# Kernel optimization log

Measured on AMD Instinct MI355X. Metric: run time of the kernel, lower is better.

## Reference

```python
import jax, jax.numpy as jnp
import numpy as np

C = 256
C8 = C // 8


def setup_inputs() -> dict:
    key = jax.random.key(0)
    ks = jax.random.split(key, 9)
    B, H, W = 4, 64, 64
    s = 1.0 / np.sqrt(C)
    return {
        "pre_feat": jax.random.normal(ks[0], (B, C, H, W), jnp.float32),
        "post_feat": jax.random.normal(ks[1], (B, C, H, W), jnp.float32),
        "Wq": jax.random.normal(ks[2], (C8, C), jnp.float32) * s,
        "bq": jnp.zeros((C8,), jnp.float32),
        "Wk": jax.random.normal(ks[3], (C8, C), jnp.float32) * s,
        "bk": jnp.zeros((C8,), jnp.float32),
        "Wv": jax.random.normal(ks[4], (C, C), jnp.float32) * s,
        "bv": jnp.zeros((C,), jnp.float32),
        "gamma": jnp.zeros((1,), jnp.float32),
    }


def reference(pre_feat, post_feat, Wq, bq, Wk, bk, Wv, bv, gamma):
    B, Cc, H, W = pre_feat.shape
    N = H * W
    pre = pre_feat.reshape(B, Cc, N)    # (B, C, N)
    post = post_feat.reshape(B, Cc, N)
    # 1x1 convs == per-pixel linear projections
    q = jnp.einsum('dc,bcn->bdn', Wq, post) + bq[None, :, None]  # (B, C8, N)
    k = jnp.einsum('dc,bcn->bdn', Wk, pre) + bk[None, :, None]   # (B, C8, N)
    v = jnp.einsum('dc,bcn->bdn', Wv, pre) + bv[None, :, None]   # (B, C, N)
    # energy[b,i,j] = <q[b,:,i], k[b,:,j]>  (unscaled)
    energy = jnp.einsum('bdi,bdj->bij', q, k)                    # (B, N, N)
    attention = jax.nn.softmax(energy, axis=-1)
    # out[b,c,i] = sum_j v[b,c,j] * attention[b,i,j]
    out = jnp.einsum('bcj,bij->bci', v, attention).reshape(B, Cc, H, W)
    return gamma[0] * out + post_feat
```

## Files before the change

kernel.cpp:

```cpp
#include <hip/hip_runtime.h>
#include <hip/hip_bf16.h>

#define Bn 4
#define Cn 256
#define Dn 32
#define Nn 4096

typedef __bf16 bf16x8 __attribute__((ext_vector_type(8)));
typedef float f32x4 __attribute__((ext_vector_type(4)));

__device__ __forceinline__ float bf2f(unsigned short u) {
  unsigned int v = ((unsigned int)u) << 16;
  return __builtin_bit_cast(float, v);
}
__device__ __forceinline__ unsigned short f2bf(float f) {
  unsigned int v = __builtin_bit_cast(unsigned int, f);
  v += 0x7FFFu + ((v >> 16) & 1u);
  return (unsigned short)(v >> 16);
}
__device__ __forceinline__ unsigned int pk2(float a, float b) {
  union { __hip_bfloat162 h; unsigned int u; } x;
  x.h = __float22bfloat162_rn(make_float2(a, b));
  return x.u;
}
__device__ __forceinline__ bf16x8 ldfrag(const unsigned short* p) {
  return __builtin_bit_cast(bf16x8, *(const uint4*)p);
}
__device__ __forceinline__ uint4 pack8(const float* p) {
  float4 a = *(const float4*)p;
  float4 b = *(const float4*)(p + 4);
  union { unsigned int u2[4]; uint4 u; } x;
  x.u2[0] = pk2(a.x, a.y); x.u2[1] = pk2(a.z, a.w);
  x.u2[2] = pk2(b.x, b.y); x.u2[3] = pk2(b.z, b.w);
  return x.u;
}
__device__ __forceinline__ void async16(unsigned short* lds, const unsigned short* g) {
  __builtin_amdgcn_global_load_lds(
      (const __attribute__((address_space(1))) unsigned int*)g,
      (__attribute__((address_space(3))) unsigned int*)lds, 16, 0, 0);
}

__global__ __launch_bounds__(256) void wconv(
    const float* __restrict__ Wq, const float* __restrict__ Wk,
    const float* __restrict__ Wv,
    unsigned short* __restrict__ WqBf, unsigned short* __restrict__ WkBf,
    unsigned short* __restrict__ WvBf)
{
  const size_t base = ((size_t)blockIdx.x * 256 + threadIdx.x) * 8;
  if (base < 8192) {
    *(uint4*)(WqBf + base) = pack8(Wq + base);
  } else if (base < 16384) {
    *(uint4*)(WkBf + base - 8192) = pack8(Wk + base - 8192);
  } else {
    *(uint4*)(WvBf + base - 16384) = pack8(Wv + base - 16384);
  }
}

#define PSTR 280
__global__ __launch_bounds__(512) void qkprep(
    const float* __restrict__ pre, const float* __restrict__ post,
    const unsigned short* __restrict__ WqBf, const float* __restrict__ bq,
    const unsigned short* __restrict__ WkBf, const float* __restrict__ bk,
    const unsigned short* __restrict__ WvBf, const float* __restrict__ bv,
    unsigned short* __restrict__ Qt, unsigned short* __restrict__ Kt,
    unsigned short* __restrict__ VBf)
{
  __shared__ __align__(16) unsigned short smem[2 * 32 * PSTR];
  unsigned short* sPre  = smem;
  unsigned short* sPost = smem + 32 * PSTR;
  unsigned short* sV    = smem;

  const int tid = threadIdx.x;
  const int lane = tid & 63, w = tid >> 6;
  const int quad = lane >> 4, n16 = lane & 15;
  const int b = blockIdx.x >> 7;
  const int i0 = (blockIdx.x & 127) << 5;
  const int isub = w & 1, role = w >> 1;
  const int i = i0 + isub * 16 + n16;

#pragma unroll
  for (int it = 0; it < 4; it++) {
    const int idx = it * 512 + tid;
    const int c = idx >> 3, ioff = (idx & 7) << 2;
    const size_t goff = ((size_t)b * Cn + c) * Nn + i0 + ioff;
    float4 vp = *(const float4*)(pre + goff);
    float4 vq = *(const float4*)(post + goff);
    sPre[(ioff + 0) * PSTR + c] = f2bf(vp.x);
    sPre[(ioff + 1) * PSTR + c] = f2bf(vp.y);
    sPre[(ioff + 2) * PSTR + c] = f2bf(vp.z);
    sPre[(ioff + 3) * PSTR + c] = f2bf(vp.w);
    sPost[(ioff + 0) * PSTR + c] = f2bf(vq.x);
    sPost[(ioff + 1) * PSTR + c] = f2bf(vq.y);
    sPost[(ioff + 2) * PSTR + c] = f2bf(vq.z);
    sPost[(ioff + 3) * PSTR + c] = f2bf(vq.w);
  }
  __syncthreads();

  const f32x4 zz = {0.f, 0.f, 0.f, 0.f};
  f32x4 aqk = zz;
  f32x4 accv[4];
#pragma unroll
  for (int ct = 0; ct < 4; ct++) accv[ct] = zz;

  const int irow = (isub * 16 + n16) * PSTR;

#pragma unroll
  for (int kc = 0; kc < 8; kc++) {
    const int co = kc * 32 + quad * 8;
    bf16x8 bq8 = ldfrag(sPre + irow + co);
    if (role < 2) {
      bf16x8 bp = ldfrag(sPost + irow + co);
      bf16x8 awq = ldfrag(WqBf + (size_t)(role * 16 + n16) * Cn + co);
      aqk = __builtin_amdgcn_mfma_f32_16x16x32_bf16(awq, bp, aqk, 0, 0, 0);
    } else {
      bf16x8 awk = ldfrag(WkBf + (size_t)((role - 2) * 16 + n16) * Cn + co);
      aqk = __builtin_amdgcn_mfma_f32_16x16x32_bf16(awk, bq8, aqk, 0, 0, 0);
    }
#pragma unroll
    for (int ct = 0; ct < 4; ct++) {
      bf16x8 aw = ldfrag(WvBf + (size_t)(role * 64 + ct * 16 + n16) * Cn + co);
      accv[ct] = __builtin_amdgcn_mfma_f32_16x16x32_bf16(aw, bq8, accv[ct], 0, 0, 0);
    }
  }

  const float LOG2E = 1.44269504f;
  if (role < 2) {
    union { unsigned short s[4]; uint2 u; } oq;
#pragma unroll
    for (int r = 0; r < 4; r++) {
      const int d = role * 16 + quad * 4 + r;
      oq.s[r] = f2bf((aqk[r] + bq[d]) * LOG2E);
    }
    *(uint2*)(Qt + ((size_t)b * Nn + i) * Dn + role * 16 + quad * 4) = oq.u;
  } else {
    union { unsigned short s[4]; uint2 u; } ok;
#pragma unroll
    for (int r = 0; r < 4; r++) {
      const int d = (role - 2) * 16 + quad * 4 + r;
      ok.s[r] = f2bf(aqk[r] + bk[d]);
    }
    *(uint2*)(Kt + ((size_t)b * Nn + i) * Dn + (role - 2) * 16 + quad * 4) = ok.u;
  }

  __syncthreads();
#pragma unroll
  for (int ct = 0; ct < 4; ct++) {
#pragma unroll
    for (int r = 0; r < 4; r++) {
      const int c = role * 64 + ct * 16 + quad * 4 + r;
      sV[c * 40 + isub * 16 + n16] = f2bf(accv[ct][r] + bv[c]);
    }
  }
  __syncthreads();
#pragma unroll
  for (int k = 0; k < 2; k++) {
    const int slot = tid + k * 512;
    const int c = slot >> 2, seg = slot & 3;
    *(uint4*)(VBf + ((size_t)b * Cn + c) * Nn + i0 + seg * 8) =
        *(const uint4*)(sV + c * 40 + seg * 8);
  }
}

__global__ __launch_bounds__(256, 4) void flash_attn(
    const unsigned short* __restrict__ Qt, const unsigned short* __restrict__ Kt,
    const unsigned short* __restrict__ VBf,
    unsigned short* __restrict__ Opart, float* __restrict__ Lpart)
{
  __shared__ __align__(16) unsigned short sX[256 * 64];
  __shared__ __align__(16) unsigned short Pl[64 * 64];

  const int tid = threadIdx.x;
  const int lane = tid & 63, w = tid >> 6;
  const int quad = lane >> 4, n16 = lane & 15;
  const int bid = blockIdx.x;
  const int pair = bid & 7, sub = bid >> 3;
  const int b  = pair >> 1;
  const int js = ((pair & 1) << 1) | (sub >> 6);
  const int it = sub & 63;
  const int i0 = it * 64;
  const int jbase = js * 1024;

  const bf16x8 qf = ldfrag(Qt + ((size_t)b * Nn + i0 + w * 16 + n16) * Dn + quad * 8);

  const f32x4 zz = {0.f, 0.f, 0.f, 0.f};
  f32x4 acc[4][4];
#pragma unroll
  for (int sub2 = 0; sub2 < 4; sub2++)
#pragma unroll
    for (int ct = 0; ct < 4; ct++) acc[sub2][ct] = zz;
  float lrow = 0.f;

  const size_t laneoff = (size_t)(lane >> 3) * Nn + (size_t)(((lane & 7) ^ (lane >> 3)) << 3);
  const unsigned short* preB = VBf + (size_t)b * Cn * Nn + laneoff;
  const int xsw = n16 & 7;
  const int xoff0 = (quad ^ xsw) << 3;
  const int xoff1 = ((4 + quad) ^ xsw) << 3;
  const int psw = (n16 & 7) << 3;

  for (int t = 0; t < 16; ++t) {
    const int j0 = jbase + t * 64;
    __syncthreads();
#pragma unroll
    for (int k = 0; k < 8; k++) {
      const int rb = (k * 4 + w) * 8;
      async16(sX + rb * 64 + (lane << 3), preB + (size_t)rb * Nn + j0);
    }
    {
      f32x4 sc[4];
#pragma unroll
      for (int jt = 0; jt < 4; jt++) {
        bf16x8 akf = ldfrag(Kt + ((size_t)b * Nn + j0 + jt * 16 + n16) * Dn + quad * 8);
        sc[jt] = __builtin_amdgcn_mfma_f32_16x16x32_bf16(akf, qf, zz, 0, 0, 0);
      }
      float ps = 0.f;
#pragma unroll
      for (int jt = 0; jt < 4; jt++) {
        float p0 = exp2f(fminf(sc[jt][0], 101.f));
        float p1 = exp2f(fminf(sc[jt][1], 101.f));
        float p2 = exp2f(fminf(sc[jt][2], 101.f));
        float p3 = exp2f(fminf(sc[jt][3], 101.f));
        ps += (p0 + p1) + (p2 + p3);
        union { unsigned int u2[2]; uint2 u; } pk;
        pk.u2[0] = pk2(p0, p1);
        pk.u2[1] = pk2(p2, p3);
        *(uint2*)&Pl[(size_t)(w * 16 + n16) * 64 + ((jt * 16 + quad * 4) ^ psw)] = pk.u;
      }
      ps += __shfl_xor(ps, 16);
      ps += __shfl_xor(ps, 32);
      lrow += ps;
    }
    __syncthreads();

    __builtin_amdgcn_s_setprio(1);
#pragma unroll
    for (int kc = 0; kc < 2; kc++) {
      const int xo = kc ? xoff1 : xoff0;
      bf16x8 pB[4];
#pragma unroll
      for (int sub2 = 0; sub2 < 4; sub2++)
        pB[sub2] = ldfrag(&Pl[(size_t)(sub2 * 16 + n16) * 64 + ((kc * 32 + quad * 8) ^ psw)]);
#pragma unroll
      for (int ct = 0; ct < 4; ct++) {
        const int crow = w * 64 + ct * 16 + n16;
        bf16x8 av = ldfrag(&sX[crow * 64 + xo]);
        acc[0][ct] = __builtin_amdgcn_mfma_f32_16x16x32_bf16(av, pB[0], acc[0][ct], 0, 0, 0);
        acc[1][ct] = __builtin_amdgcn_mfma_f32_16x16x32_bf16(av, pB[1], acc[1][ct], 0, 0, 0);
        acc[2][ct] = __builtin_amdgcn_mfma_f32_16x16x32_bf16(av, pB[2], acc[2][ct], 0, 0, 0);
        acc[3][ct] = __builtin_amdgcn_mfma_f32_16x16x32_bf16(av, pB[3], acc[3][ct], 0, 0, 0);
      }
    }
    __builtin_amdgcn_s_setprio(0);
  }

  const size_t pbase = (size_t)(js * 4 + b) * Nn;
  if (quad == 0) Lpart[pbase + i0 + w * 16 + n16] = lrow;
#pragma unroll
  for (int sub2 = 0; sub2 < 4; sub2++) {
    const int i = i0 + sub2 * 16 + n16;
#pragma unroll
    for (int ct = 0; ct < 4; ct++) {
      union { unsigned int u2[2]; uint2 u; } pk;
      pk.u2[0] = pk2(acc[sub2][ct][0], acc[sub2][ct][1]);
      pk.u2[1] = pk2(acc[sub2][ct][2], acc[sub2][ct][3]);
      *(uint2*)(Opart + (pbase + i) * 256 + w * 64 + ct * 16 + quad * 4) = pk.u;
    }
  }
}

__global__ __launch_bounds__(256) void combine(
    const unsigned short* __restrict__ Opart, const float* __restrict__ Lpart,
    const float* __restrict__ post, const float* __restrict__ gamma,
    float* __restrict__ out)
{
  __shared__ float sT[64 * 65];
  __shared__ float sL[64];

  const int tid = threadIdx.x;
  const int b = blockIdx.x >> 8;
  const int rest = blockIdx.x & 255;
  const int i0 = (rest >> 2) * 64;
  const int c0 = (rest & 3) * 64;

  if (tid < 64) {
    float l = 0.f;
#pragma unroll
    for (int js = 0; js < 4; js++) l += Lpart[(size_t)(js * 4 + b) * Nn + i0 + tid];
    sL[tid] = 1.f / l;
  }
  __syncthreads();

#pragma unroll
  for (int pass = 0; pass < 2; pass++) {
    const int il = (tid >> 3) + pass * 32;
    const int c8 = (tid & 7) << 3;
    float a[8] = {0.f, 0.f, 0.f, 0.f, 0.f, 0.f, 0.f, 0.f};
#pragma unroll
    for (int js = 0; js < 4; js++) {
      uint4 uu = *(const uint4*)(Opart + ((size_t)(js * 4 + b) * Nn + i0 + il) * 256 + c0 + c8);
      const unsigned short* us = (const unsigned short*)&uu;
#pragma unroll
      for (int e = 0; e < 8; e++) a[e] += bf2f(us[e]);
    }
    const float inv = sL[il];
#pragma unroll
    for (int e = 0; e < 8; e++) sT[(c8 + e) * 65 + il] = a[e] * inv;
  }
  __syncthreads();

  const float g = gamma[0];
#pragma unroll
  for (int itr = 0; itr < 4; itr++) {
    const int slot = tid + itr * 256;
    const int cr = slot >> 4, i4 = (slot & 15) << 2;
    const size_t addr = ((size_t)b * Cn + c0 + cr) * Nn + i0 + i4;
    float4 pp = *(const float4*)(post + addr);
    float4 ov;
    ov.x = g * sT[cr * 65 + i4 + 0] + pp.x;
    ov.y = g * sT[cr * 65 + i4 + 1] + pp.y;
    ov.z = g * sT[cr * 65 + i4 + 2] + pp.z;
    ov.w = g * sT[cr * 65 + i4 + 3] + pp.w;
    *(float4*)(out + addr) = ov;
  }
}

extern "C" void kernel_launch(void* const* d_in, const int* in_sizes, int n_in,
                              void* d_out, int out_size, void* d_ws, size_t ws_size,
                              hipStream_t stream) {
  const float* pre   = (const float*)d_in[0];
  const float* post  = (const float*)d_in[1];
  const float* Wq    = (const float*)d_in[2];
  const float* bq    = (const float*)d_in[3];
  const float* Wk    = (const float*)d_in[4];
  const float* bk    = (const float*)d_in[5];
  const float* Wv    = (const float*)d_in[6];
  const float* bv    = (const float*)d_in[7];
  const float* gamma = (const float*)d_in[8];
  float* out = (float*)d_out;

  unsigned short* ws = (unsigned short*)d_ws;
  unsigned short* Qt    = ws;
  unsigned short* Kt    = Qt + (size_t)Bn * Nn * Dn;
  unsigned short* VBf   = Kt + (size_t)Bn * Nn * Dn;
  unsigned short* WqBf  = VBf + (size_t)Bn * Cn * Nn;
  unsigned short* WkBf  = WqBf + Dn * Cn;
  unsigned short* WvBf  = WkBf + Dn * Cn;
  float* Lpart = (float*)(WvBf + Cn * Cn);
  unsigned short* Opart = (unsigned short*)(Lpart + 4 * Bn * Nn);

  wconv<<<40, 256, 0, stream>>>(Wq, Wk, Wv, WqBf, WkBf, WvBf);
  qkprep<<<512, 512, 0, stream>>>(pre, post, WqBf, bq, WkBf, bk, WvBf, bv,
                                  Qt, Kt, VBf);
  flash_attn<<<1024, 256, 0, stream>>>(Qt, Kt, VBf, Opart, Lpart);
  combine<<<1024, 256, 0, stream>>>(Opart, Lpart, post, gamma, out);
}
```

Before: 180.4 us.

## Halve qkprep pixel tile to 16 and launch twice as many blocks

The projection prep kernel now handles 16 pixels per block instead of 32, with 1024 blocks and a smaller shared-memory footprint. The warp role mapping changes so that all 8 warps each compute 32 V channels, while only 4 warps compute Q/K. The aim is more blocks in flight and better occupancy on the memory-bound projection stage (launch bounds now request 8 waves per EU). In exchange, weight fragments are reloaded by twice as many blocks, half the warps sit idle during the Q/K part, and global stores to VBf are shorter (32 bytes per channel row).

After: 185.0 us. 2.5% more time.

```diff
diff --git a/kernel.cpp b/kernel.cpp
--- a/kernel.cpp
+++ b/kernel.cpp
@@ -57,7 +57,7 @@
 }
 
 #define PSTR 280
-__global__ __launch_bounds__(512) void qkprep(
+__global__ __launch_bounds__(512, 8) void qkprep(
     const float* __restrict__ pre, const float* __restrict__ post,
     const unsigned short* __restrict__ WqBf, const float* __restrict__ bq,
     const unsigned short* __restrict__ WkBf, const float* __restrict__ bk,
@@ -65,23 +65,23 @@
     unsigned short* __restrict__ Qt, unsigned short* __restrict__ Kt,
     unsigned short* __restrict__ VBf)
 {
-  __shared__ __align__(16) unsigned short smem[2 * 32 * PSTR];
+  __shared__ __align__(16) unsigned short smem[2 * 16 * PSTR];
   unsigned short* sPre  = smem;
-  unsigned short* sPost = smem + 32 * PSTR;
+  unsigned short* sPost = smem + 16 * PSTR;
   unsigned short* sV    = smem;
 
   const int tid = threadIdx.x;
   const int lane = tid & 63, w = tid >> 6;
   const int quad = lane >> 4, n16 = lane & 15;
-  const int b = blockIdx.x >> 7;
-  const int i0 = (blockIdx.x & 127) << 5;
-  const int isub = w & 1, role = w >> 1;
-  const int i = i0 + isub * 16 + n16;
-
-#pragma unroll
-  for (int it = 0; it < 4; it++) {
+  const int b = blockIdx.x >> 8;
+  const int i0 = (blockIdx.x & 255) << 4;
+  const int i = i0 + n16;
+  const int dh = w & 1;
+
+#pragma unroll
+  for (int it = 0; it < 2; it++) {
     const int idx = it * 512 + tid;
-    const int c = idx >> 3, ioff = (idx & 7) << 2;
+    const int c = idx >> 2, ioff = (idx & 3) << 2;
     const size_t goff = ((size_t)b * Cn + c) * Nn + i0 + ioff;
     float4 vp = *(const float4*)(pre + goff);
     float4 vq = *(const float4*)(post + goff);
@@ -98,66 +98,59 @@
 
   const f32x4 zz = {0.f, 0.f, 0.f, 0.f};
   f32x4 aqk = zz;
-  f32x4 accv[4];
-#pragma unroll
-  for (int ct = 0; ct < 4; ct++) accv[ct] = zz;
-
-  const int irow = (isub * 16 + n16) * PSTR;
+  f32x4 accv0 = zz, accv1 = zz;
+  const int irow = n16 * PSTR;
 
 #pragma unroll
   for (int kc = 0; kc < 8; kc++) {
     const int co = kc * 32 + quad * 8;
     bf16x8 bq8 = ldfrag(sPre + irow + co);
-    if (role < 2) {
+    if (w < 2) {
       bf16x8 bp = ldfrag(sPost + irow + co);
-      bf16x8 awq = ldfrag(WqBf + (size_t)(role * 16 + n16) * Cn + co);
+      bf16x8 awq = ldfrag(WqBf + (size_t)(dh * 16 + n16) * Cn + co);
       aqk = __builtin_amdgcn_mfma_f32_16x16x32_bf16(awq, bp, aqk, 0, 0, 0);
-    } else {
-      bf16x8 awk = ldfrag(WkBf + (size_t)((role - 2) * 16 + n16) * Cn + co);
+    } else if (w < 4) {
+      bf16x8 awk = ldfrag(WkBf + (size_t)(dh * 16 + n16) * Cn + co);
       aqk = __builtin_amdgcn_mfma_f32_16x16x32_bf16(awk, bq8, aqk, 0, 0, 0);
     }
-#pragma unroll
-    for (int ct = 0; ct < 4; ct++) {
-      bf16x8 aw = ldfrag(WvBf + (size_t)(role * 64 + ct * 16 + n16) * Cn + co);
-      accv[ct] = __builtin_amdgcn_mfma_f32_16x16x32_bf16(aw, bq8, accv[ct], 0, 0, 0);
-    }
+    bf16x8 aw0 = ldfrag(WvBf + (size_t)(w * 32 + n16) * Cn + co);
+    bf16x8 aw1 = ldfrag(WvBf + (size_t)(w * 32 + 16 + n16) * Cn + co);
+    accv0 = __builtin_amdgcn_mfma_f32_16x16x32_bf16(aw0, bq8, accv0, 0, 0, 0);
+    accv1 = __builtin_amdgcn_mfma_f32_16x16x32_bf16(aw1, bq8, accv1, 0, 0, 0);
   }
 
   const float LOG2E = 1.44269504f;
-  if (role < 2) {
+  if (w < 2) {
     union { unsigned short s[4]; uint2 u; } oq;
 #pragma unroll
     for (int r = 0; r < 4; r++) {
-      const int d = role * 16 + quad * 4 + r;
+      const int d = dh * 16 + quad * 4 + r;
       oq.s[r] = f2bf((aqk[r] + bq[d]) * LOG2E);
     }
-    *(uint2*)(Qt + ((size_t)b * Nn + i) * Dn + role * 16 + quad * 4) = oq.u;
-  } else {
+    *(uint2*)(Qt + ((size_t)b * Nn + i) * Dn + dh * 16 + quad * 4) = oq.u;
+  } else if (w < 4) {
     union { unsigned short s[4]; uint2 u; } ok;
 #pragma unroll
     for (int r = 0; r < 4; r++) {
-      const int d = (role - 2) * 16 + quad * 4 + r;
+      const int d = dh * 16 + quad * 4 + r;
       ok.s[r] = f2bf(aqk[r] + bk[d]);
     }
-    *(uint2*)(Kt + ((size_t)b * Nn + i) * Dn + (role - 2) * 16 + quad * 4) = ok.u;
-  }
-
-  __syncthreads();
-#pragma unroll
-  for (int ct = 0; ct < 4; ct++) {
-#pragma unroll
-    for (int r = 0; r < 4; r++) {
-      const int c = role * 64 + ct * 16 + quad * 4 + r;
-      sV[c * 40 + isub * 16 + n16] = f2bf(accv[ct][r] + bv[c]);
-    }
-  }
-  __syncthreads();
-#pragma unroll
-  for (int k = 0; k < 2; k++) {
-    const int slot = tid + k * 512;
-    const int c = slot >> 2, seg = slot & 3;
+    *(uint2*)(Kt + ((size_t)b * Nn + i) * Dn + dh * 16 + quad * 4) = ok.u;
+  }
+
+  __syncthreads();
+#pragma unroll
+  for (int r = 0; r < 4; r++) {
+    const int c0v = w * 32 + quad * 4 + r;
+    sV[c0v * 24 + n16] = f2bf(accv0[r] + bv[c0v]);
+    const int c1v = w * 32 + 16 + quad * 4 + r;
+    sV[c1v * 24 + n16] = f2bf(accv1[r] + bv[c1v]);
+  }
+  __syncthreads();
+  {
+    const int c = tid >> 1, seg = tid & 1;
     *(uint4*)(VBf + ((size_t)b * Cn + c) * Nn + i0 + seg * 8) =
-        *(const uint4*)(sV + c * 40 + seg * 8);
+        *(const uint4*)(sV + c * 24 + seg * 8);
   }
 }
 
@@ -348,8 +341,8 @@
   unsigned short* Opart = (unsigned short*)(Lpart + 4 * Bn * Nn);
 
   wconv<<<40, 256, 0, stream>>>(Wq, Wk, Wv, WqBf, WkBf, WvBf);
-  qkprep<<<512, 512, 0, stream>>>(pre, post, WqBf, bq, WkBf, bk, WvBf, bv,
-                                  Qt, Kt, VBf);
+  qkprep<<<1024, 512, 0, stream>>>(pre, post, WqBf, bq, WkBf, bk, WvBf, bv,
+                                   Qt, Kt, VBf);
   flash_attn<<<1024, 256, 0, stream>>>(Qt, Kt, VBf, Opart, Lpart);
   combine<<<1024, 256, 0, stream>>>(Opart, Lpart, post, gamma, out);
 }
```
